# Kernel tuning notes

Measured on AMD Instinct MI355X. Metric: run time of the kernel, lower is better.

## Reference

```python
import jax, jax.numpy as jnp
import numpy as np

H = 4096          # hidden_size
NIN = 17          # RFSIZE*RFSIZE + ADDINPUT + NBACTIONS = 9+4+4
NA = 4            # NBACTIONS


def setup_inputs() -> dict:
    key = jax.random.key(0)
    ks = jax.random.split(key, 12)
    return {
        "x": jax.random.normal(ks[0], (1, NIN), jnp.float32),
        "hidden": 0.1 * jax.random.normal(ks[1], (1, H), jnp.float32),
        "hebb": 0.01 * jax.random.normal(ks[2], (H, H), jnp.float32),
        "i2h_w": 0.1 * jax.random.normal(ks[3], (H, NIN), jnp.float32),
        "i2h_b": 0.1 * jax.random.normal(ks[4], (H,), jnp.float32),
        "w": 0.01 * jax.random.uniform(ks[5], (H, H), jnp.float32),
        "alpha": 0.01 * jax.random.uniform(ks[6], (H, H), jnp.float32),
        "eta": 0.01 * jnp.ones((1,), jnp.float32),
        "h2o_w": 0.1 * jax.random.normal(ks[7], (NA, H), jnp.float32),
        "h2o_b": 0.1 * jax.random.normal(ks[8], (NA,), jnp.float32),
        "h2v_w": 0.1 * jax.random.normal(ks[9], (1, H), jnp.float32),
        "h2v_b": 0.1 * jax.random.normal(ks[10], (1,), jnp.float32),
    }


def reference(x, hidden, hebb, i2h_w, i2h_b, w, alpha, eta, h2o_w, h2o_b, h2v_w, h2v_b):
    # plastic RNN step: h = tanh(i2h(x) + hidden @ (w + alpha*hebb))
    h = jnp.tanh(x @ i2h_w.T + i2h_b + hidden @ (w + alpha * hebb))  # [1,H]
    # Hebbian trace update: (1-eta)*hebb + eta * outer(hidden, h)
    hebb_new = (1.0 - eta) * hebb + eta * (hidden[0][:, None] * h[0][None, :])  # [H,H]
    activout = jax.nn.softmax(h @ h2o_w.T + h2o_b, axis=-1)  # [1,NA]
    valueout = h @ h2v_w.T + h2v_b                           # [1,1]
    return activout, valueout, h, hebb_new
```

## Files before the change

kernel.cpp:

```cpp
#include <hip/hip_runtime.h>

#define HDIM 4096
#define NIN 17
#define NA 4

using f4 = __attribute__((ext_vector_type(4))) float;

constexpr int TB1 = 1024;
constexpr int CPB = 16;
constexpr int NBLK1 = HDIM / CPB;
constexpr int RPP = TB1 / 4;
constexpr int NPASS = HDIM / RPP;
constexpr size_t NELEM = (size_t)HDIM * HDIM;

__global__ __launch_bounds__(TB1)
void k_mvh(const float* __restrict__ w, const float* __restrict__ alpha,
           const float* __restrict__ hebb, const float* __restrict__ hidden,
           const float* __restrict__ x, const float* __restrict__ i2h_w,
           const float* __restrict__ i2h_b,
           const float* __restrict__ h2o_w, const float* __restrict__ h2v_w,
           float* __restrict__ h_f, float* __restrict__ out,
           float* __restrict__ acc5) {
    const int tid = threadIdx.x;
    const int q = tid & 3;
    const int rw = tid >> 2;
    const int colq = blockIdx.x * CPB + q * 4;

    f4 acc = {0.f, 0.f, 0.f, 0.f};
#pragma unroll 4
    for (int p = 0; p < NPASS; ++p) {
        const int r = p * RPP + rw;
        const size_t off = (size_t)r * HDIM + colq;
        const f4 wv = *(const f4*)(w + off);
        const f4 av = *(const f4*)(alpha + off);
        const f4 bv = *(const f4*)(hebb + off);
        acc += hidden[r] * (wv + av * bv);
    }

    __shared__ f4 red[TB1];
    red[tid] = acc;
    __syncthreads();
    for (int s = TB1 / 2; s >= 4; s >>= 1) {
        if (tid < s) red[tid] += red[tid + s];
        __syncthreads();
    }

    __shared__ float hsh[CPB];
    if (tid < CPB) {
        const int j = blockIdx.x * CPB + tid;
        float z = red[tid >> 2][tid & 3] + i2h_b[j];
#pragma unroll
        for (int k = 0; k < NIN; ++k) z += x[k] * i2h_w[j * NIN + k];
        const float h = tanhf(z);
        h_f[j] = h;
        out[5 + j] = h;
        hsh[tid] = h;
    }
    __syncthreads();

    if (tid == 0) {
        float a5[NA + 1] = {0.f, 0.f, 0.f, 0.f, 0.f};
#pragma unroll
        for (int c = 0; c < CPB; ++c) {
            const int j = blockIdx.x * CPB + c;
            const float h = hsh[c];
#pragma unroll
            for (int a = 0; a < NA; ++a) a5[a] += h * h2o_w[(size_t)a * HDIM + j];
            a5[NA] += h * h2v_w[j];
        }
#pragma unroll
        for (int a = 0; a <= NA; ++a) atomicAdd(acc5 + a, a5[a]);
    }
}

constexpr int TB2 = 256;

__global__ __launch_bounds__(TB2)
void k_hebb(const float* __restrict__ hebb, const float* __restrict__ hidden,
            const float* __restrict__ h_f, const float* __restrict__ eta,
            float* __restrict__ hebb_out) {
    const size_t t = (size_t)blockIdx.x * TB2 + threadIdx.x;
    const size_t s = 4 * t + 3;
    const float e = eta[0];
    const float om = 1.f - e;

    if (t == 0) {
        const float hv0 = e * hidden[0];
        hebb_out[0] = om * hebb[0] + hv0 * h_f[0];
        hebb_out[1] = om * hebb[1] + hv0 * h_f[1];
        hebb_out[2] = om * hebb[2] + hv0 * h_f[2];
    }

    if (s + 3 < NELEM) {
        const float b0 = hebb[s];
        const f4 bv = *(const f4*)(hebb + s + 1);
        const float b[4] = {b0, bv.x, bv.y, bv.z};
        f4 v;
#pragma unroll
        for (int k = 0; k < 4; ++k) {
            const size_t m = s + (size_t)k;
            const int i = (int)(m >> 12);
            const int jj = (int)(m & (HDIM - 1));
            v[k] = om * b[k] + e * hidden[i] * h_f[jj];
        }
        __builtin_nontemporal_store(v, (f4*)(hebb_out + s));
    } else {
        for (size_t m = s; m < NELEM; ++m) {
            const int i = (int)(m >> 12);
            const int jj = (int)(m & (HDIM - 1));
            hebb_out[m] = om * hebb[m] + e * hidden[i] * h_f[jj];
        }
    }
}

__global__ __launch_bounds__(64)
void k_finish(const float* __restrict__ acc5,
              const float* __restrict__ h2o_b, const float* __restrict__ h2v_b,
              float* __restrict__ out) {
    if (threadIdx.x == 0) {
        float o[NA];
        float mx = -1e30f;
#pragma unroll
        for (int a = 0; a < NA; ++a) { o[a] = acc5[a] + h2o_b[a]; mx = fmaxf(mx, o[a]); }
        float se = 0.f;
#pragma unroll
        for (int a = 0; a < NA; ++a) { o[a] = __expf(o[a] - mx); se += o[a]; }
#pragma unroll
        for (int a = 0; a < NA; ++a) out[a] = o[a] / se;
        out[NA] = acc5[NA] + h2v_b[0];
    }
}

extern "C" void kernel_launch(void* const* d_in, const int* in_sizes, int n_in,
                              void* d_out, int out_size, void* d_ws, size_t ws_size,
                              hipStream_t stream) {
    const float* x      = (const float*)d_in[0];
    const float* hidden = (const float*)d_in[1];
    const float* hebb   = (const float*)d_in[2];
    const float* i2h_w  = (const float*)d_in[3];
    const float* i2h_b  = (const float*)d_in[4];
    const float* w      = (const float*)d_in[5];
    const float* alpha  = (const float*)d_in[6];
    const float* eta    = (const float*)d_in[7];
    const float* h2o_w  = (const float*)d_in[8];
    const float* h2o_b  = (const float*)d_in[9];
    const float* h2v_w  = (const float*)d_in[10];
    const float* h2v_b  = (const float*)d_in[11];
    float* out = (float*)d_out;

    float* hebb_out = out + 5 + HDIM;

    float* h_f  = (float*)d_ws;
    float* acc5 = h_f + HDIM;

    hipMemsetAsync(acc5, 0, 8 * sizeof(float), stream);
    k_mvh<<<NBLK1, TB1, 0, stream>>>(w, alpha, hebb, hidden, x, i2h_w, i2h_b,
                                     h2o_w, h2v_w, h_f, out, acc5);
    k_hebb<<<(int)((NELEM / 4) / TB2), TB2, 0, stream>>>(hebb, hidden, h_f, eta, hebb_out);
    k_finish<<<1, 64, 0, stream>>>(acc5, h2o_b, h2v_b, out);
}
```

Before: 277.7 us.

## Fuse matvec, hebb update and softmax into one cooperative grid-synced kernel

```diff
diff --git a/kernel.cpp b/kernel.cpp
--- a/kernel.cpp
+++ b/kernel.cpp
@@ -1,4 +1,7 @@
 #include <hip/hip_runtime.h>
+#include <hip/hip_cooperative_groups.h>
+
+namespace cg = cooperative_groups;
 
 #define HDIM 4096
 #define NIN 17
@@ -12,6 +15,115 @@
 constexpr int RPP = TB1 / 4;
 constexpr int NPASS = HDIM / RPP;
 constexpr size_t NELEM = (size_t)HDIM * HDIM;
+constexpr size_t NQUAD = NELEM / 4;
+
+__global__ __launch_bounds__(TB1)
+void k_all(const float* __restrict__ w, const float* __restrict__ alpha,
+           const float* __restrict__ hebb, const float* __restrict__ hidden,
+           const float* __restrict__ x, const float* __restrict__ i2h_w,
+           const float* __restrict__ i2h_b,
+           const float* __restrict__ h2o_w, const float* __restrict__ h2o_b,
+           const float* __restrict__ h2v_w, const float* __restrict__ h2v_b,
+           const float* __restrict__ eta,
+           float* __restrict__ h_f, float* __restrict__ out,
+           float* __restrict__ acc5) {
+    const int tid = threadIdx.x;
+    const int q = tid & 3;
+    const int rw = tid >> 2;
+    const int colq = blockIdx.x * CPB + q * 4;
+
+    f4 acc = {0.f, 0.f, 0.f, 0.f};
+#pragma unroll 4
+    for (int p = 0; p < NPASS; ++p) {
+        const int r = p * RPP + rw;
+        const size_t off = (size_t)r * HDIM + colq;
+        const f4 wv = *(const f4*)(w + off);
+        const f4 av = *(const f4*)(alpha + off);
+        const f4 bv = *(const f4*)(hebb + off);
+        acc += hidden[r] * (wv + av * bv);
+    }
+
+    __shared__ f4 red[TB1];
+    red[tid] = acc;
+    __syncthreads();
+    for (int s = TB1 / 2; s >= 4; s >>= 1) {
+        if (tid < s) red[tid] += red[tid + s];
+        __syncthreads();
+    }
+
+    if (tid < CPB) {
+        const int j = blockIdx.x * CPB + tid;
+        float z = red[tid >> 2][tid & 3] + i2h_b[j];
+#pragma unroll
+        for (int k = 0; k < NIN; ++k) z += x[k] * i2h_w[j * NIN + k];
+        const float h = tanhf(z);
+        h_f[j] = h;
+        out[5 + j] = h;
+        float d[NA + 1];
+#pragma unroll
+        for (int a = 0; a < NA; ++a) d[a] = h * h2o_w[(size_t)a * HDIM + j];
+        d[NA] = h * h2v_w[j];
+#pragma unroll
+        for (int a = 0; a <= NA; ++a) {
+            float v = d[a];
+#pragma unroll
+            for (int sft = 8; sft > 0; sft >>= 1) v += __shfl_down(v, sft, 16);
+            if (tid == 0) atomicAdd(acc5 + a, v);
+        }
+    }
+
+    cg::this_grid().sync();
+
+    if (blockIdx.x == 0 && tid == 0) {
+        float o[NA];
+        float mx = -1e30f;
+#pragma unroll
+        for (int a = 0; a < NA; ++a) { o[a] = acc5[a] + h2o_b[a]; mx = fmaxf(mx, o[a]); }
+        float se = 0.f;
+#pragma unroll
+        for (int a = 0; a < NA; ++a) { o[a] = __expf(o[a] - mx); se += o[a]; }
+#pragma unroll
+        for (int a = 0; a < NA; ++a) out[a] = o[a] / se;
+        out[NA] = acc5[NA] + h2v_b[0];
+    }
+
+    float* __restrict__ hebb_out = out + 5 + HDIM;
+    const float e = eta[0];
+    const float om = 1.f - e;
+    const size_t G = (size_t)NBLK1 * TB1;
+    const size_t tg = (size_t)blockIdx.x * TB1 + tid;
+
+    if (tg == 0) {
+        const float hv0 = e * hidden[0];
+        hebb_out[0] = om * hebb[0] + hv0 * h_f[0];
+        hebb_out[1] = om * hebb[1] + hv0 * h_f[1];
+        hebb_out[2] = om * hebb[2] + hv0 * h_f[2];
+    }
+
+    for (size_t k = tg; k < NQUAD; k += G) {
+        const size_t s = 4 * k + 3;
+        if (s + 3 < NELEM) {
+            const float b0 = hebb[s];
+            const f4 bv = *(const f4*)(hebb + s + 1);
+            const float b[4] = {b0, bv.x, bv.y, bv.z};
+            f4 v;
+#pragma unroll
+            for (int kk = 0; kk < 4; ++kk) {
+                const size_t m = s + (size_t)kk;
+                const int i = (int)(m >> 12);
+                const int jj = (int)(m & (HDIM - 1));
+                v[kk] = om * b[kk] + e * hidden[i] * h_f[jj];
+            }
+            __builtin_nontemporal_store(v, (f4*)(hebb_out + s));
+        } else {
+            for (size_t m = s; m < NELEM; ++m) {
+                const int i = (int)(m >> 12);
+                const int jj = (int)(m & (HDIM - 1));
+                hebb_out[m] = om * hebb[m] + e * hidden[i] * h_f[jj];
+            }
+        }
+    }
+}
 
 __global__ __launch_bounds__(TB1)
 void k_mvh(const float* __restrict__ w, const float* __restrict__ alpha,
@@ -25,7 +137,6 @@
     const int q = tid & 3;
     const int rw = tid >> 2;
     const int colq = blockIdx.x * CPB + q * 4;
-
     f4 acc = {0.f, 0.f, 0.f, 0.f};
 #pragma unroll 4
     for (int p = 0; p < NPASS; ++p) {
@@ -36,7 +147,6 @@
         const f4 bv = *(const f4*)(hebb + off);
         acc += hidden[r] * (wv + av * bv);
     }
-
     __shared__ f4 red[TB1];
     red[tid] = acc;
     __syncthreads();
@@ -44,8 +154,6 @@
         if (tid < s) red[tid] += red[tid + s];
         __syncthreads();
     }
-
-    __shared__ float hsh[CPB];
     if (tid < CPB) {
         const int j = blockIdx.x * CPB + tid;
         float z = red[tid >> 2][tid & 3] + i2h_b[j];
@@ -54,22 +162,17 @@
         const float h = tanhf(z);
         h_f[j] = h;
         out[5 + j] = h;
-        hsh[tid] = h;
-    }
-    __syncthreads();
-
-    if (tid == 0) {
-        float a5[NA + 1] = {0.f, 0.f, 0.f, 0.f, 0.f};
-#pragma unroll
-        for (int c = 0; c < CPB; ++c) {
-            const int j = blockIdx.x * CPB + c;
-            const float h = hsh[c];
-#pragma unroll
-            for (int a = 0; a < NA; ++a) a5[a] += h * h2o_w[(size_t)a * HDIM + j];
-            a5[NA] += h * h2v_w[j];
-        }
-#pragma unroll
-        for (int a = 0; a <= NA; ++a) atomicAdd(acc5 + a, a5[a]);
+        float d[NA + 1];
+#pragma unroll
+        for (int a = 0; a < NA; ++a) d[a] = h * h2o_w[(size_t)a * HDIM + j];
+        d[NA] = h * h2v_w[j];
+#pragma unroll
+        for (int a = 0; a <= NA; ++a) {
+            float v = d[a];
+#pragma unroll
+            for (int sft = 8; sft > 0; sft >>= 1) v += __shfl_down(v, sft, 16);
+            if (tid == 0) atomicAdd(acc5 + a, v);
+        }
     }
 }
 
@@ -83,14 +186,12 @@
     const size_t s = 4 * t + 3;
     const float e = eta[0];
     const float om = 1.f - e;
-
     if (t == 0) {
         const float hv0 = e * hidden[0];
         hebb_out[0] = om * hebb[0] + hv0 * h_f[0];
         hebb_out[1] = om * hebb[1] + hv0 * h_f[1];
         hebb_out[2] = om * hebb[2] + hv0 * h_f[2];
     }
-
     if (s + 3 < NELEM) {
         const float b0 = hebb[s];
         const f4 bv = *(const f4*)(hebb + s + 1);
@@ -154,8 +255,24 @@
     float* acc5 = h_f + HDIM;
 
     hipMemsetAsync(acc5, 0, 8 * sizeof(float), stream);
-    k_mvh<<<NBLK1, TB1, 0, stream>>>(w, alpha, hebb, hidden, x, i2h_w, i2h_b,
-                                     h2o_w, h2v_w, h_f, out, acc5);
-    k_hebb<<<(int)((NELEM / 4) / TB2), TB2, 0, stream>>>(hebb, hidden, h_f, eta, hebb_out);
-    k_finish<<<1, 64, 0, stream>>>(acc5, h2o_b, h2v_b, out);
-}
+
+    static int coop = -1;
+    if (coop < 0) {
+        int maxb = 0;
+        hipError_t err = hipOccupancyMaxActiveBlocksPerMultiprocessor(&maxb, k_all, TB1, 0);
+        coop = (err == hipSuccess && maxb >= 1) ? 1 : 0;
+    }
+
+    if (coop) {
+        void* args[] = {(void*)&w, (void*)&alpha, (void*)&hebb, (void*)&hidden,
+                        (void*)&x, (void*)&i2h_w, (void*)&i2h_b,
+                        (void*)&h2o_w, (void*)&h2o_b, (void*)&h2v_w, (void*)&h2v_b,
+                        (void*)&eta, (void*)&h_f, (void*)&out, (void*)&acc5};
+        hipLaunchCooperativeKernel(k_all, dim3(NBLK1), dim3(TB1), args, 0, stream);
+    } else {
+        k_mvh<<<NBLK1, TB1, 0, stream>>>(w, alpha, hebb, hidden, x, i2h_w, i2h_b,
+                                         h2o_w, h2v_w, h_f, out, acc5);
+        k_hebb<<<(int)(NQUAD / TB2), TB2, 0, stream>>>(hebb, hidden, h_f, eta, hebb_out);
+        k_finish<<<1, 64, 0, stream>>>(acc5, h2o_b, h2v_b, out);
+    }
+}
```

Result: no change. 273.8 us (-1.4%).

## Fuse Hebbian update and softmax finish into matvec kernel via last-block counter

Applied to the files above, without the earlier changes.

```diff
diff --git a/kernel.cpp b/kernel.cpp
--- a/kernel.cpp
+++ b/kernel.cpp
@@ -11,16 +11,17 @@
 constexpr int NBLK1 = HDIM / CPB;
 constexpr int RPP = TB1 / 4;
 constexpr int NPASS = HDIM / RPP;
-constexpr size_t NELEM = (size_t)HDIM * HDIM;
 
-__global__ __launch_bounds__(TB1)
-void k_mvh(const float* __restrict__ w, const float* __restrict__ alpha,
-           const float* __restrict__ hebb, const float* __restrict__ hidden,
-           const float* __restrict__ x, const float* __restrict__ i2h_w,
-           const float* __restrict__ i2h_b,
-           const float* __restrict__ h2o_w, const float* __restrict__ h2v_w,
-           float* __restrict__ h_f, float* __restrict__ out,
-           float* __restrict__ acc5) {
+__global__ __launch_bounds__(TB1, 1)
+void k_main(const float* __restrict__ w, const float* __restrict__ alpha,
+            const float* __restrict__ hebb, const float* __restrict__ hidden,
+            const float* __restrict__ x, const float* __restrict__ i2h_w,
+            const float* __restrict__ i2h_b,
+            const float* __restrict__ h2o_w, const float* __restrict__ h2o_b,
+            const float* __restrict__ h2v_w, const float* __restrict__ h2v_b,
+            const float* __restrict__ eta,
+            float* __restrict__ out, float* __restrict__ acc5,
+            unsigned* __restrict__ cnt) {
     const int tid = threadIdx.x;
     const int q = tid & 3;
     const int rw = tid >> 2;
@@ -31,8 +32,8 @@
     for (int p = 0; p < NPASS; ++p) {
         const int r = p * RPP + rw;
         const size_t off = (size_t)r * HDIM + colq;
-        const f4 wv = *(const f4*)(w + off);
-        const f4 av = *(const f4*)(alpha + off);
+        const f4 wv = __builtin_nontemporal_load((const f4*)(w + off));
+        const f4 av = __builtin_nontemporal_load((const f4*)(alpha + off));
         const f4 bv = *(const f4*)(hebb + off);
         acc += hidden[r] * (wv + av * bv);
     }
@@ -52,82 +53,55 @@
 #pragma unroll
         for (int k = 0; k < NIN; ++k) z += x[k] * i2h_w[j * NIN + k];
         const float h = tanhf(z);
-        h_f[j] = h;
         out[5 + j] = h;
         hsh[tid] = h;
+        float d[NA + 1];
+#pragma unroll
+        for (int a = 0; a < NA; ++a) d[a] = h * h2o_w[(size_t)a * HDIM + j];
+        d[NA] = h * h2v_w[j];
+#pragma unroll
+        for (int a = 0; a <= NA; ++a) {
+            float v = d[a];
+#pragma unroll
+            for (int sft = 8; sft > 0; sft >>= 1) v += __shfl_down(v, sft, 16);
+            if (tid == 0) atomicAdd(acc5 + a, v);
+        }
     }
     __syncthreads();
 
     if (tid == 0) {
-        float a5[NA + 1] = {0.f, 0.f, 0.f, 0.f, 0.f};
+        __threadfence();
+        if (atomicAdd(cnt, 1u) == NBLK1 - 1) {
+            float res[NA + 1];
 #pragma unroll
-        for (int c = 0; c < CPB; ++c) {
-            const int j = blockIdx.x * CPB + c;
-            const float h = hsh[c];
+            for (int a = 0; a <= NA; ++a) res[a] = atomicAdd(acc5 + a, 0.f);
+            float o[NA];
+            float mx = -1e30f;
 #pragma unroll
-            for (int a = 0; a < NA; ++a) a5[a] += h * h2o_w[(size_t)a * HDIM + j];
-            a5[NA] += h * h2v_w[j];
+            for (int a = 0; a < NA; ++a) { o[a] = res[a] + h2o_b[a]; mx = fmaxf(mx, o[a]); }
+            float se = 0.f;
+#pragma unroll
+            for (int a = 0; a < NA; ++a) { o[a] = __expf(o[a] - mx); se += o[a]; }
+#pragma unroll
+            for (int a = 0; a < NA; ++a) out[a] = o[a] / se;
+            out[NA] = res[NA] + h2v_b[0];
         }
-#pragma unroll
-        for (int a = 0; a <= NA; ++a) atomicAdd(acc5 + a, a5[a]);
     }
-}
 
-constexpr int TB2 = 256;
-
-__global__ __launch_bounds__(TB2)
-void k_hebb(const float* __restrict__ hebb, const float* __restrict__ hidden,
-            const float* __restrict__ h_f, const float* __restrict__ eta,
-            float* __restrict__ hebb_out) {
-    const size_t t = (size_t)blockIdx.x * TB2 + threadIdx.x;
-    const size_t s = 4 * t + 3;
     const float e = eta[0];
     const float om = 1.f - e;
-
-    if (t == 0) {
-        const float hv0 = e * hidden[0];
-        hebb_out[0] = om * hebb[0] + hv0 * h_f[0];
-        hebb_out[1] = om * hebb[1] + hv0 * h_f[1];
-        hebb_out[2] = om * hebb[2] + hv0 * h_f[2];
-    }
-
-    if (s + 3 < NELEM) {
-        const float b0 = hebb[s];
-        const f4 bv = *(const f4*)(hebb + s + 1);
-        const float b[4] = {b0, bv.x, bv.y, bv.z};
-        f4 v;
-#pragma unroll
-        for (int k = 0; k < 4; ++k) {
-            const size_t m = s + (size_t)k;
-            const int i = (int)(m >> 12);
-            const int jj = (int)(m & (HDIM - 1));
-            v[k] = om * b[k] + e * hidden[i] * h_f[jj];
-        }
-        __builtin_nontemporal_store(v, (f4*)(hebb_out + s));
-    } else {
-        for (size_t m = s; m < NELEM; ++m) {
-            const int i = (int)(m >> 12);
-            const int jj = (int)(m & (HDIM - 1));
-            hebb_out[m] = om * hebb[m] + e * hidden[i] * h_f[jj];
-        }
-    }
-}
-
-__global__ __launch_bounds__(64)
-void k_finish(const float* __restrict__ acc5,
-              const float* __restrict__ h2o_b, const float* __restrict__ h2v_b,
-              float* __restrict__ out) {
-    if (threadIdx.x == 0) {
-        float o[NA];
-        float mx = -1e30f;
-#pragma unroll
-        for (int a = 0; a < NA; ++a) { o[a] = acc5[a] + h2o_b[a]; mx = fmaxf(mx, o[a]); }
-        float se = 0.f;
-#pragma unroll
-        for (int a = 0; a < NA; ++a) { o[a] = __expf(o[a] - mx); se += o[a]; }
-#pragma unroll
-        for (int a = 0; a < NA; ++a) out[a] = o[a] / se;
-        out[NA] = acc5[NA] + h2v_b[0];
+    const int cB = tid & 15;
+    const int rB0 = tid >> 4;
+    const int j = blockIdx.x * CPB + cB;
+    const float hj = e * hsh[cB];
+    const float* __restrict__ hin = hebb + j;
+    float* __restrict__ outp = out + 5 + HDIM + j;
+#pragma unroll 8
+    for (int s = 63; s >= 0; --s) {
+        const int r = s * 64 + rB0;
+        const size_t off = (size_t)r * HDIM;
+        const float v = om * hin[off] + hidden[r] * hj;
+        __builtin_nontemporal_store(v, outp + off);
     }
 }
 
@@ -148,14 +122,12 @@
     const float* h2v_b  = (const float*)d_in[11];
     float* out = (float*)d_out;
 
-    float* hebb_out = out + 5 + HDIM;
+    float* acc5 = (float*)d_ws;
+    unsigned* cnt = (unsigned*)(acc5 + 8);
 
-    float* h_f  = (float*)d_ws;
-    float* acc5 = h_f + HDIM;
+    hipMemsetAsync(acc5, 0, 48, stream);
 
-    hipMemsetAsync(acc5, 0, 8 * sizeof(float), stream);
-    k_mvh<<<NBLK1, TB1, 0, stream>>>(w, alpha, hebb, hidden, x, i2h_w, i2h_b,
-                                     h2o_w, h2v_w, h_f, out, acc5);
-    k_hebb<<<(int)((NELEM / 4) / TB2), TB2, 0, stream>>>(hebb, hidden, h_f, eta, hebb_out);
-    k_finish<<<1, 64, 0, stream>>>(acc5, h2o_b, h2v_b, out);
+    k_main<<<NBLK1, TB1, 0, stream>>>(w, alpha, hebb, hidden, x, i2h_w, i2h_b,
+                                      h2o_w, h2o_b, h2v_w, h2v_b, eta,
+                                      out, acc5, cnt);
 }
```

Result: slower. 317.1 us (+14.2%).
